# Optimization experiments

Hardware: AMD Instinct MI355X
Metric: run time of the kernel (lower is better)

Reference implementation:

```python
import jax, jax.numpy as jnp
import numpy as np
import math

B, T, D = 4, 4096, 512
K_CACHE = 16

def _layernorm(x, g, b, eps=1e-5):
    mu = x.mean(-1, keepdims=True)
    var = ((x - mu) ** 2).mean(-1, keepdims=True)
    return (x - mu) / jnp.sqrt(var + eps) * g + b

def _shift1(x):
    # prepend zero along time axis, drop last: x_prev[t] = x[t-1]
    return jnp.pad(x, ((0, 0), (1, 0), (0, 0)))[:, :-1]

def mipt_parallel_scan(p, theta, inp_re, inp_im):
    # Faithful replication of the torch loop: ceil(log2(T+1)) iterations,
    # each combining with the element shifted by ONE position (as written).
    Bt, Tt, Dt = p.shape
    a_re = (1.0 - p) * jnp.cos(theta)
    a_im = (1.0 - p) * jnp.sin(theta)
    b_re, b_im = inp_re, inp_im
    mask = (jnp.arange(Tt) >= 1)[None, :, None]
    steps = math.ceil(math.log2(Tt + 1))
    for _ in range(steps):
        ar_p, ai_p = _shift1(a_re), _shift1(a_im)
        br_p, bi_p = _shift1(b_re), _shift1(b_im)
        new_a_re = a_re * ar_p - a_im * ai_p
        new_a_im = a_re * ai_p + a_im * ar_p
        new_b_re = a_re * br_p - a_im * bi_p + b_re
        new_b_im = a_re * bi_p + a_im * br_p + b_im
        a_re = jnp.where(mask, new_a_re, a_re)
        a_im = jnp.where(mask, new_a_im, a_im)
        b_re = jnp.where(mask, new_b_re, b_re)
        b_im = jnp.where(mask, new_b_im, b_im)
    return b_re, b_im

def setup_inputs() -> dict:
    key = jax.random.key(0)
    ks = jax.random.split(key, 32)
    s = 0.02
    def W(k, i, o):
        return jax.random.normal(k, (i, o), jnp.float32) * s
    inp = {
        'x': jax.random.normal(ks[0], (B, T, D), jnp.float32),
        'ln1_g': jnp.ones((D,), jnp.float32), 'ln1_b': jnp.zeros((D,), jnp.float32),
        'ln2_g': jnp.ones((D,), jnp.float32), 'ln2_b': jnp.zeros((D,), jnp.float32),
        'Wp_w': W(ks[1], D, D), 'Wp_b': jnp.zeros((D,), jnp.float32),
        'Wt_w': W(ks[2], D, D), 'Wt_b': jnp.zeros((D,), jnp.float32),
        'Wr_w': W(ks[3], D, D), 'Wr_b': jnp.zeros((D,), jnp.float32),
        'Wi_w': W(ks[4], D, D), 'Wi_b': jnp.zeros((D,), jnp.float32),
        'Wk_w': W(ks[5], D, D), 'Wk_b': jnp.zeros((D,), jnp.float32),
        'Wv_w': W(ks[6], D, D), 'Wv_b': jnp.zeros((D,), jnp.float32),
        'Wq_w': W(ks[7], D, D), 'Wq_b': jnp.zeros((D,), jnp.float32),
        'gate_w': W(ks[8], D, 1), 'gate_b': jnp.zeros((1,), jnp.float32),
        'ffn1_w': W(ks[9], D, 4 * D), 'ffn1_b': jnp.zeros((4 * D,), jnp.float32),
        'ffn2_w': W(ks[10], 4 * D, D), 'ffn2_b': jnp.zeros((D,), jnp.float32),
    }
    return inp

def reference(x, ln1_g, ln1_b, ln2_g, ln2_b, Wp_w, Wp_b, Wt_w, Wt_b, Wr_w, Wr_b,
              Wi_w, Wi_b, Wk_w, Wk_b, Wv_w, Wv_b, Wq_w, Wq_b, gate_w, gate_b,
              ffn1_w, ffn1_b, ffn2_w, ffn2_b):
    Bx, Tx, Dx = x.shape
    residual = x
    xn = _layernorm(x, ln1_g, ln1_b)
    p = jax.nn.sigmoid(xn @ Wp_w + Wp_b)
    theta = xn @ Wt_w + Wt_b
    inp_re = xn @ Wr_w + Wr_b
    inp_im = xn @ Wi_w + Wi_b
    h_re, _h_im = mipt_parallel_scan(p, theta, inp_re, inp_im)
    h_mean = h_re.mean(axis=1)  # [B, D]
    # CausalSparseCache (eval mode)
    p_scalar = p.mean(axis=-1)  # [B, T]
    K = min(K_CACHE, Tx)
    _, topk_idx = jax.lax.top_k(p_scalar, K)  # [B, K]
    idx = jnp.broadcast_to(topk_idx[:, :, None], (Bx, K, Dx))
    h_topk = jnp.take_along_axis(h_re, idx, axis=1)  # [B, K, D]
    keys = h_topk @ Wk_w + Wk_b
    values = h_topk @ Wv_w + Wv_b
    query = (h_mean @ Wq_w + Wq_b)[:, None, :]  # [B, 1, D]
    scores = jnp.einsum('bqd,bkd->bqk', query, keys) / math.sqrt(Dx)
    attn = jax.nn.softmax(scores, axis=-1)
    cache_out = jnp.einsum('bqk,bkd->bqd', attn, values)[:, 0]  # [B, D]
    g = jax.nn.sigmoid(h_mean @ gate_w + gate_b)  # [B, 1]
    out = h_mean + g * cache_out
    h = h_re + residual
    hn = _layernorm(h, ln2_g, ln2_b)
    ffn = jax.nn.gelu(hn @ ffn1_w + ffn1_b, approximate=False) @ ffn2_w + ffn2_b
    h = h + ffn
    return (h, out)
```

## Files before the change

kernel.cpp:

```cpp
#include <hip/hip_runtime.h>
#include <hip/hip_bf16.h>
#include <cstdint>
#include <cstddef>

typedef __bf16 bf16;
typedef __attribute__((ext_vector_type(8))) __bf16 bf16x8;
typedef __attribute__((ext_vector_type(4))) float f32x4;

#define BB 4
#define TT 4096
#define DD 512
#define MM (BB * TT)
#define OUT1_OFF ((size_t)MM * DD)

typedef __attribute__((address_space(1))) void as1_void;
typedef __attribute__((address_space(3))) void as3_void;

__device__ __forceinline__ void gl_lds16(const void* g, void* l) {
    __builtin_amdgcn_global_load_lds((as1_void*)(uintptr_t)g,
                                     (as3_void*)(uintptr_t)l, 16, 0, 0);
}

__global__ void transpose_bf16(const float* __restrict__ in, bf16* __restrict__ out,
                               int R, int C) {
    __shared__ float tile[32][33];
    const int c0 = blockIdx.x * 32, r0 = blockIdx.y * 32;
    const int tx = threadIdx.x, ty = threadIdx.y;
#pragma unroll
    for (int i = 0; i < 32; i += 8)
        tile[ty + i][tx] = in[(size_t)(r0 + ty + i) * C + (c0 + tx)];
    __syncthreads();
#pragma unroll
    for (int i = 0; i < 32; i += 8)
        out[(size_t)(c0 + ty + i) * R + (r0 + tx)] = (bf16)tile[tx][ty + i];
}

__global__ void pack_bias(const float* __restrict__ a, const float* __restrict__ b,
                          const float* __restrict__ c, const float* __restrict__ d,
                          float* __restrict__ o) {
    const int i = blockIdx.x * 256 + threadIdx.x;
    if (i < 2048) {
        const float* s = (i < 512) ? a : (i < 1024) ? b : (i < 1536) ? c : d;
        o[i] = s[i & 511];
    }
}

__global__ void zero_kernel(float* __restrict__ p, int n) {
    const int i = blockIdx.x * 256 + threadIdx.x;
    if (i < n) p[i] = 0.f;
}

__global__ __launch_bounds__(256) void ln_kernel(
    const float* __restrict__ X, const float* __restrict__ Xadd,
    const float* __restrict__ gw, const float* __restrict__ bw,
    bf16* __restrict__ out) {
    const int row = blockIdx.x * 4 + (threadIdx.x >> 6);
    const int lane = threadIdx.x & 63;
    const float* xr = X + (size_t)row * DD + lane * 8;
    float v[8];
    float4 v0 = *(const float4*)xr;
    float4 v1 = *(const float4*)(xr + 4);
    v[0] = v0.x; v[1] = v0.y; v[2] = v0.z; v[3] = v0.w;
    v[4] = v1.x; v[5] = v1.y; v[6] = v1.z; v[7] = v1.w;
    if (Xadd) {
        const float* ad = Xadd + (size_t)row * DD + lane * 8;
        float4 a0 = *(const float4*)ad;
        float4 a1 = *(const float4*)(ad + 4);
        v[0] += a0.x; v[1] += a0.y; v[2] += a0.z; v[3] += a0.w;
        v[4] += a1.x; v[5] += a1.y; v[6] += a1.z; v[7] += a1.w;
    }
    float s = 0.f, ss = 0.f;
#pragma unroll
    for (int i = 0; i < 8; ++i) { s += v[i]; ss += v[i] * v[i]; }
#pragma unroll
    for (int o = 32; o; o >>= 1) { s += __shfl_down(s, o); ss += __shfl_down(ss, o); }
    s = __shfl(s, 0); ss = __shfl(ss, 0);
    const float mu = s * (1.f / DD);
    const float var = ss * (1.f / DD) - mu * mu;
    const float rstd = rsqrtf(var + 1e-5f);
    bf16x8 o8;
#pragma unroll
    for (int i = 0; i < 8; ++i)
        o8[i] = (bf16)((v[i] - mu) * rstd * gw[lane * 8 + i] + bw[lane * 8 + i]);
    *(bf16x8*)(out + (size_t)row * DD + lane * 8) = o8;
}

#define MF(a_, b_, c_) c_ = __builtin_amdgcn_mfma_f32_16x16x32_bf16(a_, b_, c_, 0, 0, 0)

template <int MODE>
__global__ __launch_bounds__(256) void gemm_bt(
    const bf16* __restrict__ A, const bf16* __restrict__ Bt,
    const float* __restrict__ bias, void* __restrict__ Cout,
    void* __restrict__ Cout2,
    const float* __restrict__ add1, const float* __restrict__ add2,
    int M, int N, int K) {
    __shared__ bf16 As[2][4096];
    __shared__ bf16 Bs[2][4096];
    const int tid = threadIdx.x;
    const int lane = tid & 63;
    const int wv = tid >> 6;
    const int wr = wv >> 1, wc = wv & 1;
    const int nb = N >> 7;
    const int nwg = gridDim.x;
    int bx = blockIdx.x;
    if ((nwg & 7) == 0) bx = (bx & 7) * (nwg >> 3) + (bx >> 3);
    const int bm = bx / nb, bn = bx % nb;
    const int m0 = bm << 7, n0 = bn << 7;

    const int srow = tid >> 2;
    const int scol = (((tid & 3) ^ ((tid >> 3) & 3)) << 3);
    const bf16* Asrc = A + (size_t)(m0 + srow) * K + scol;
    const bf16* Bsrc = Bt + (size_t)(n0 + srow) * K + scol;
    const size_t rstep = (size_t)64 * K;

    const int lr = lane & 15, lg = lane >> 4;
    const int sel = ((lg ^ ((lr >> 1) & 3)) << 3);
    const int aoff = (wr * 64 + lr) * 32 + sel;
    const int boff = (wc * 64 + lr) * 32 + sel;

#define STG(buf, k0)                                                \
    do {                                                            \
        gl_lds16(Asrc + (k0),         &As[buf][wv * 512]);          \
        gl_lds16(Asrc + (k0) + rstep, &As[buf][wv * 512 + 2048]);   \
        gl_lds16(Bsrc + (k0),         &Bs[buf][wv * 512]);          \
        gl_lds16(Bsrc + (k0) + rstep, &Bs[buf][wv * 512 + 2048]);   \
    } while (0)

    f32x4 acc00 = {}, acc01 = {}, acc02 = {}, acc03 = {};
    f32x4 acc10 = {}, acc11 = {}, acc12 = {}, acc13 = {};
    f32x4 acc20 = {}, acc21 = {}, acc22 = {}, acc23 = {};
    f32x4 acc30 = {}, acc31 = {}, acc32 = {}, acc33 = {};

    const int NT = K >> 5;
    STG(0, 0);
    STG(1, 32);
    for (int t = 0; t < NT; ++t) {
        if (t + 1 < NT) asm volatile("s_waitcnt vmcnt(4)" ::: "memory");
        else            asm volatile("s_waitcnt vmcnt(0)" ::: "memory");
        __builtin_amdgcn_s_barrier();
        asm volatile("" ::: "memory");
        const bf16* Ab = As[t & 1];
        const bf16* Bb = Bs[t & 1];
        bf16x8 af0 = *(const bf16x8*)&Ab[aoff];
        bf16x8 af1 = *(const bf16x8*)&Ab[aoff + 512];
        bf16x8 af2 = *(const bf16x8*)&Ab[aoff + 1024];
        bf16x8 af3 = *(const bf16x8*)&Ab[aoff + 1536];
        bf16x8 bf0 = *(const bf16x8*)&Bb[boff];
        bf16x8 bf1 = *(const bf16x8*)&Bb[boff + 512];
        bf16x8 bf2 = *(const bf16x8*)&Bb[boff + 1024];
        bf16x8 bf3 = *(const bf16x8*)&Bb[boff + 1536];
        MF(af0, bf0, acc00); MF(af0, bf1, acc01); MF(af0, bf2, acc02); MF(af0, bf3, acc03);
        MF(af1, bf0, acc10); MF(af1, bf1, acc11); MF(af1, bf2, acc12); MF(af1, bf3, acc13);
        MF(af2, bf0, acc20); MF(af2, bf1, acc21); MF(af2, bf2, acc22); MF(af2, bf3, acc23);
        MF(af3, bf0, acc30); MF(af3, bf1, acc31); MF(af3, bf2, acc32); MF(af3, bf3, acc33);
        __builtin_amdgcn_s_barrier();
        asm volatile("" ::: "memory");
        if (t + 2 < NT) STG(t & 1, (t + 2) << 5);
    }
#undef STG

#define EPI(mi, ni, ACC)                                                        \
    do {                                                                        \
        const int gmb = m0 + wr * 64 + mi * 16 + 4 * lg;                        \
        const int gn = n0 + wc * 64 + ni * 16 + lr;                             \
        const float bia = bias[gn];                                             \
        _Pragma("unroll")                                                       \
        for (int i = 0; i < 4; ++i) {                                           \
            float v = ACC[i] + bia;                                             \
            const int row = gmb + i;                                            \
            if (MODE == 0) {                                                    \
                if (gn < 512) ((float*)Cout)[(size_t)row * 512 + gn] = v;       \
                else ((bf16*)Cout2)[(size_t)row * 1536 + (gn - 512)] = (bf16)v; \
            } else if (MODE == 1) {                                             \
                const float ge = 0.5f * v * (1.0f + erff(v * 0.70710678118654752f)); \
                ((bf16*)Cout)[(size_t)row * N + gn] = (bf16)ge;                 \
            } else {                                                            \
                const size_t off = (size_t)row * N + gn;                        \
                ((float*)Cout)[off] = v + add1[off] + add2[off];                \
            }                                                                   \
        }                                                                       \
    } while (0)
    EPI(0, 0, acc00); EPI(0, 1, acc01); EPI(0, 2, acc02); EPI(0, 3, acc03);
    EPI(1, 0, acc10); EPI(1, 1, acc11); EPI(1, 2, acc12); EPI(1, 3, acc13);
    EPI(2, 0, acc20); EPI(2, 1, acc21); EPI(2, 2, acc22); EPI(2, 3, acc23);
    EPI(3, 0, acc30); EPI(3, 1, acc31); EPI(3, 2, acc32); EPI(3, 3, acc33);
#undef EPI
}

__global__ __launch_bounds__(256) void pscalar_kernel(const float* __restrict__ linp,
                                                      float* __restrict__ ps) {
    const int row = blockIdx.x * 4 + (threadIdx.x >> 6);
    const int lane = threadIdx.x & 63;
    const float* pr = linp + (size_t)row * 512 + lane * 8;
    float s = 0.f;
#pragma unroll
    for (int i = 0; i < 8; ++i) {
        const float v = pr[i];
        s += __builtin_amdgcn_rcpf(1.f + __expf(-v));
    }
#pragma unroll
    for (int o = 32; o; o >>= 1) s += __shfl_down(s, o);
    if (!lane) ps[row] = s * (1.f / 512.f);
}

#define SCL 16
__global__ __launch_bounds__(256) void scan_kernel(const float* __restrict__ linp,
                                                   const bf16* __restrict__ lint,
                                                   float* __restrict__ h_re) {
    const int blk = blockIdx.x;
    const int dh = blk & 1;
    const int tc = (blk >> 1) & 255;
    const int b = blk >> 9;
    const int d = dh * 256 + threadIdx.x;
    const int t0 = tc * SCL;

    float par[13], pai[13], pbr[13], pbi[13];
#pragma unroll
    for (int k = 0; k < 13; ++k) { par[k] = 0.f; pai[k] = 0.f; pbr[k] = 0.f; pbi[k] = 0.f; }

    const int warm = (tc == 0) ? 0 : 13;
    const float* pp = linp + (size_t)(b * TT + t0 - warm) * 512 + d;
    const bf16* tp = lint + (size_t)(b * TT + t0 - warm) * 1536 + d;
    float* pout = h_re + ((size_t)(b * TT + t0)) * DD + d;

#define XFORM(car, cai, cbr, cbi)                                        \
    const float pl = pp[0];                                              \
    const float th = (float)tp[0];                                       \
    const float re = (float)tp[512];                                     \
    const float im = (float)tp[1024];                                    \
    pp += 512; tp += 1536;                                               \
    const float om = __builtin_amdgcn_rcpf(1.f + __expf(pl));            \
    float fr_, sn, cs;                                                   \
    { const float rv_ = th * 0.15915494309189535f;                       \
      asm("v_fract_f32 %0, %1" : "=v"(fr_) : "v"(rv_));                  \
      asm("v_sin_f32 %0, %1" : "=v"(sn) : "v"(fr_));                     \
      asm("v_cos_f32 %0, %1" : "=v"(cs) : "v"(fr_)); }                   \
    float car = om * cs, cai = om * sn, cbr = re, cbi = im;

    for (int s = 0; s < warm; ++s) {
        XFORM(car, cai, cbr, cbi)
#pragma unroll
        for (int k = 0; k < 13; ++k) {
            const float tar = par[k], tai = pai[k], tbr = pbr[k], tbi = pbi[k];
            par[k] = car; pai[k] = cai; pbr[k] = cbr; pbi[k] = cbi;
            const float nbr = car * tbr - cai * tbi + cbr;
            const float nbi = car * tbi + cai * tbr + cbi;
            if (k < 12) {
                const float nar = car * tar - cai * tai;
                const float nai = car * tai + cai * tar;
                car = nar; cai = nai;
            }
            cbr = nbr; cbi = nbi;
        }
    }

#pragma unroll 4
    for (int s = 0; s < SCL; ++s) {
        const int t = t0 + s;
        XFORM(car, cai, cbr, cbi)
        if (t == 0) {
#pragma unroll
            for (int k = 0; k < 13; ++k) { par[k] = car; pai[k] = cai; pbr[k] = cbr; pbi[k] = cbi; }
        } else {
#pragma unroll
            for (int k = 0; k < 13; ++k) {
                const float tar = par[k], tai = pai[k], tbr = pbr[k], tbi = pbi[k];
                par[k] = car; pai[k] = cai; pbr[k] = cbr; pbi[k] = cbi;
                const float nbr = car * tbr - cai * tbi + cbr;
                const float nbi = car * tbi + cai * tbr + cbi;
                if (k < 12) {
                    const float nar = car * tar - cai * tai;
                    const float nai = car * tai + cai * tar;
                    car = nar; cai = nai;
                }
                cbr = nbr; cbi = nbi;
            }
        }
        pout[(size_t)s * DD] = cbr;
    }
#undef XFORM
}

__global__ __launch_bounds__(256) void hmean_kernel(const float* __restrict__ h_re,
                                                    float* __restrict__ hsum) {
    const int blk = blockIdx.x;
    const int b = blk >> 6;
    const int dh = (blk >> 5) & 1;
    const int tc = blk & 31;
    const int d = dh * 256 + threadIdx.x;
    float s = 0.f;
    const float* p = h_re + ((size_t)(b * TT + tc * 128)) * DD + d;
    for (int t = 0; t < 128; ++t) s += p[(size_t)t * DD];
    atomicAdd(&hsum[b * DD + d], s);
}

__global__ __launch_bounds__(256) void topk_kernel(const float* __restrict__ ps,
                                                   int* __restrict__ idx_out) {
    __shared__ float vals[TT];
    __shared__ float rv[4];
    __shared__ int ri[4];
    const int b = blockIdx.x, tid = threadIdx.x;
    for (int i = tid; i < TT; i += 256) vals[i] = ps[b * TT + i];
    __syncthreads();
    for (int kk = 0; kk < 16; ++kk) {
        float bv = -1e30f; int bi = 0x7fffffff;
        for (int i = tid; i < TT; i += 256) {
            const float v = vals[i];
            if (v > bv || (v == bv && i < bi)) { bv = v; bi = i; }
        }
#pragma unroll
        for (int o = 32; o; o >>= 1) {
            const float ov = __shfl_down(bv, o);
            const int oi = __shfl_down(bi, o);
            if (ov > bv || (ov == bv && oi < bi)) { bv = ov; bi = oi; }
        }
        const int lane = tid & 63, wid = tid >> 6;
        if (!lane) { rv[wid] = bv; ri[wid] = bi; }
        __syncthreads();
        if (!tid) {
            float fbv = rv[0]; int fbi = ri[0];
            for (int w = 1; w < 4; ++w)
                if (rv[w] > fbv || (rv[w] == fbv && ri[w] < fbi)) { fbv = rv[w]; fbi = ri[w]; }
            idx_out[b * 16 + kk] = fbi;
            vals[fbi] = -1e30f;
        }
        __syncthreads();
    }
}

__global__ __launch_bounds__(256) void kv_kernel(
    const float* __restrict__ h_re, const int* __restrict__ tki,
    const float* __restrict__ Wk, const float* __restrict__ Wkb,
    const float* __restrict__ Wv, const float* __restrict__ Wvb,
    float* __restrict__ keys, float* __restrict__ vals) {
    const int blk = blockIdx.x;
    const int b = blk >> 4, j = blk & 15;
    const int tid = threadIdx.x;
    __shared__ float hrow[512];
    const int row = tki[b * 16 + j];
    for (int i = tid; i < 512; i += 256)
        hrow[i] = h_re[((size_t)(b * TT + row)) * DD + i];
    __syncthreads();
    for (int n = tid; n < 512; n += 256) {
        float sk = Wkb[n], sv = Wvb[n];
        for (int k = 0; k < 512; ++k) {
            const float h = hrow[k];
            sk += h * Wk[(size_t)k * 512 + n];
            sv += h * Wv[(size_t)k * 512 + n];
        }
        keys[((size_t)(b * 16 + j)) * 512 + n] = sk;
        vals[((size_t)(b * 16 + j)) * 512 + n] = sv;
    }
}

__global__ __launch_bounds__(256) void attn_out_kernel(
    const float* __restrict__ hsum, const float* __restrict__ Wq,
    const float* __restrict__ Wqb, const float* __restrict__ gw,
    const float* __restrict__ gb, const float* __restrict__ keys,
    const float* __restrict__ vals, float* __restrict__ out1) {
    const int b = blockIdx.x, tid = threadIdx.x;
    const int lane = tid & 63, wid = tid >> 6;
    __shared__ float hm[512];
    __shared__ float q[512];
    __shared__ float sc[16];
    __shared__ float red[4];
    for (int d0 = tid; d0 < 512; d0 += 256)
        hm[d0] = hsum[b * 512 + d0] * (1.f / 4096.f);
    __syncthreads();
    for (int n = tid; n < 512; n += 256) {
        float s = Wqb[n];
        for (int k = 0; k < 512; ++k) s += hm[k] * Wq[(size_t)k * 512 + n];
        q[n] = s;
    }
    float gp = 0.f;
    for (int k = tid; k < 512; k += 256) gp += hm[k] * gw[k];
#pragma unroll
    for (int o = 32; o; o >>= 1) gp += __shfl_down(gp, o);
    if (!lane) red[wid] = gp;
    __syncthreads();
    const float g = 1.f / (1.f + __expf(-(red[0] + red[1] + red[2] + red[3] + gb[0])));
    for (int kk = wid; kk < 16; kk += 4) {
        float sp = 0.f;
        const float* kr = keys + ((size_t)(b * 16 + kk)) * 512;
        for (int k2 = lane; k2 < 512; k2 += 64) sp += q[k2] * kr[k2];
#pragma unroll
        for (int o = 32; o; o >>= 1) sp += __shfl_down(sp, o);
        if (!lane) sc[kk] = sp * 0.04419417382415922f;
    }
    __syncthreads();
    float mx = sc[0];
#pragma unroll
    for (int kk = 1; kk < 16; ++kk) mx = fmaxf(mx, sc[kk]);
    float den = 0.f;
    float w16[16];
#pragma unroll
    for (int kk = 0; kk < 16; ++kk) { w16[kk] = __expf(sc[kk] - mx); den += w16[kk]; }
    const float rden = 1.f / den;
    for (int d0 = tid; d0 < 512; d0 += 256) {
        float co = 0.f;
#pragma unroll
        for (int kk = 0; kk < 16; ++kk)
            co += w16[kk] * vals[((size_t)(b * 16 + kk)) * 512 + d0];
        out1[b * 512 + d0] = hm[d0] + g * (co * rden);
    }
}

extern "C" void kernel_launch(void* const* d_in, const int* in_sizes, int n_in,
                              void* d_out, int out_size, void* d_ws, size_t ws_size,
                              hipStream_t stream) {
    const float* x    = (const float*)d_in[0];
    const float* ln1g = (const float*)d_in[1];
    const float* ln1b = (const float*)d_in[2];
    const float* ln2g = (const float*)d_in[3];
    const float* ln2b = (const float*)d_in[4];
    const float* Wp_w = (const float*)d_in[5];
    const float* Wp_b = (const float*)d_in[6];
    const float* Wt_w = (const float*)d_in[7];
    const float* Wt_b = (const float*)d_in[8];
    const float* Wr_w = (const float*)d_in[9];
    const float* Wr_b = (const float*)d_in[10];
    const float* Wi_w = (const float*)d_in[11];
    const float* Wi_b = (const float*)d_in[12];
    const float* Wk_w = (const float*)d_in[13];
    const float* Wk_b = (const float*)d_in[14];
    const float* Wv_w = (const float*)d_in[15];
    const float* Wv_b = (const float*)d_in[16];
    const float* Wq_w = (const float*)d_in[17];
    const float* Wq_b = (const float*)d_in[18];
    const float* gw   = (const float*)d_in[19];
    const float* gb   = (const float*)d_in[20];
    const float* f1w  = (const float*)d_in[21];
    const float* f1b  = (const float*)d_in[22];
    const float* f2w  = (const float*)d_in[23];
    const float* f2b  = (const float*)d_in[24];

    char* wsp = (char*)d_ws;
    float* linp = (float*)wsp;
    bf16* lint = (bf16*)(wsp + 33554432);
    char* p = wsp + 83886080;
    float* h_re = (float*)p; p += 33554432;
    bf16* xn = (bf16*)p;     p += 16777216;
    bf16* hn = (bf16*)p;     p += 16777216;
    bf16* wcat = (bf16*)p;   p += 2097152;
    bf16* f1bt = (bf16*)p;   p += 2097152;
    bf16* f2bt = (bf16*)p;   p += 2097152;
    float* bcat = (float*)p; p += 8192;
    float* ps = (float*)p;   p += 65536;
    float* hsum = (float*)p; p += 8192;
    int* tki = (int*)p;      p += 256;
    float* keys = (float*)p; p += 131072;
    float* valsb = (float*)p;
    bf16* act = (bf16*)wsp;
    float* out0 = (float*)d_out;
    float* out1 = (float*)d_out + OUT1_OFF;

    dim3 tb(32, 8);
    transpose_bf16<<<dim3(16, 16), tb, 0, stream>>>(Wp_w, wcat + (size_t)0 * 512 * 512, 512, 512);
    transpose_bf16<<<dim3(16, 16), tb, 0, stream>>>(Wt_w, wcat + (size_t)1 * 512 * 512, 512, 512);
    transpose_bf16<<<dim3(16, 16), tb, 0, stream>>>(Wr_w, wcat + (size_t)2 * 512 * 512, 512, 512);
    transpose_bf16<<<dim3(16, 16), tb, 0, stream>>>(Wi_w, wcat + (size_t)3 * 512 * 512, 512, 512);
    transpose_bf16<<<dim3(64, 16), tb, 0, stream>>>(f1w, f1bt, 512, 2048);
    transpose_bf16<<<dim3(16, 64), tb, 0, stream>>>(f2w, f2bt, 2048, 512);
    pack_bias<<<8, 256, 0, stream>>>(Wp_b, Wt_b, Wr_b, Wi_b, bcat);

    ln_kernel<<<4096, 256, 0, stream>>>(x, nullptr, ln1g, ln1b, xn);
    gemm_bt<0><<<2048, 256, 0, stream>>>(xn, wcat, bcat, linp, lint, nullptr, nullptr, MM, 2048, 512);
    pscalar_kernel<<<4096, 256, 0, stream>>>(linp, ps);
    scan_kernel<<<2048, 256, 0, stream>>>(linp, lint, h_re);
    zero_kernel<<<8, 256, 0, stream>>>(hsum, 2048);
    hmean_kernel<<<256, 256, 0, stream>>>(h_re, hsum);
    topk_kernel<<<4, 256, 0, stream>>>(ps, tki);
    kv_kernel<<<64, 256, 0, stream>>>(h_re, tki, Wk_w, Wk_b, Wv_w, Wv_b, keys, valsb);
    attn_out_kernel<<<4, 256, 0, stream>>>(hsum, Wq_w, Wq_b, gw, gb, keys, valsb, out1);
    ln_kernel<<<4096, 256, 0, stream>>>(h_re, x, ln2g, ln2b, hn);
    gemm_bt<1><<<2048, 256, 0, stream>>>(hn, f1bt, f1b, act, nullptr, nullptr, nullptr, MM, 2048, 512);
    gemm_bt<2><<<512, 256, 0, stream>>>(act, f2bt, f2b, out0, nullptr, h_re, x, MM, 512, 2048);
}
```

Before: 428.2 us.

## Fuse sigmoid and p-mean into projection GEMM epilogue, interleave scan inputs

Result: faster. 419.5 us (-2.0%).

```diff
diff --git a/kernel.cpp b/kernel.cpp
--- a/kernel.cpp
+++ b/kernel.cpp
@@ -5,6 +5,7 @@
 
 typedef __bf16 bf16;
 typedef __attribute__((ext_vector_type(8))) __bf16 bf16x8;
+typedef __attribute__((ext_vector_type(4))) __bf16 bf16x4;
 typedef __attribute__((ext_vector_type(4))) float f32x4;
 
 #define BB 4
@@ -20,6 +21,8 @@
     __builtin_amdgcn_global_load_lds((as1_void*)(uintptr_t)g,
                                      (as3_void*)(uintptr_t)l, 16, 0, 0);
 }
+
+#define SIGM(x) (__builtin_amdgcn_rcpf(1.f + __expf(-(x))))
 
 __global__ void transpose_bf16(const float* __restrict__ in, bf16* __restrict__ out,
                                int R, int C) {
@@ -159,6 +162,58 @@
     }
 #undef STG
 
+    if constexpr (MODE == 0) {
+        const int cls = n0 >> 9;
+        if (cls == 0) {
+            const int pidx = (n0 + wc * 64) >> 6;
+#define EPI0(mi, A0, A1, A2, A3)                                              \
+    do {                                                                      \
+        const int gmb = m0 + wr * 64 + mi * 16 + 4 * lg;                      \
+        const int dbase = n0 + wc * 64 + lr;                                  \
+        const float b0_ = bias[dbase], b1_ = bias[dbase + 16],                \
+                    b2_ = bias[dbase + 32], b3_ = bias[dbase + 48];           \
+        _Pragma("unroll")                                                     \
+        for (int i = 0; i < 4; ++i) {                                         \
+            const int row = gmb + i;                                          \
+            const float p0 = SIGM(A0[i] + b0_);                               \
+            const float p1 = SIGM(A1[i] + b1_);                               \
+            const float p2 = SIGM(A2[i] + b2_);                               \
+            const float p3 = SIGM(A3[i] + b3_);                               \
+            bf16* ob = (bf16*)Cout + (size_t)row * 2048;                      \
+            ob[(size_t)dbase * 4]        = (bf16)(1.f - p0);                  \
+            ob[(size_t)(dbase + 16) * 4] = (bf16)(1.f - p1);                  \
+            ob[(size_t)(dbase + 32) * 4] = (bf16)(1.f - p2);                  \
+            ob[(size_t)(dbase + 48) * 4] = (bf16)(1.f - p3);                  \
+            float s_ = p0 + p1 + p2 + p3;                                     \
+            s_ += __shfl_xor(s_, 1); s_ += __shfl_xor(s_, 2);                 \
+            s_ += __shfl_xor(s_, 4); s_ += __shfl_xor(s_, 8);                 \
+            if (lr == 0) ((float*)Cout2)[(size_t)pidx * MM + row] = s_;       \
+        }                                                                     \
+    } while (0)
+            EPI0(0, acc00, acc01, acc02, acc03);
+            EPI0(1, acc10, acc11, acc12, acc13);
+            EPI0(2, acc20, acc21, acc22, acc23);
+            EPI0(3, acc30, acc31, acc32, acc33);
+#undef EPI0
+        } else {
+#define EPIS(mi, ni, ACC)                                                     \
+    do {                                                                      \
+        const int gmb = m0 + wr * 64 + mi * 16 + 4 * lg;                      \
+        const int gn = n0 + wc * 64 + ni * 16 + lr;                           \
+        const int dn = gn & 511;                                              \
+        const float bia = bias[gn];                                           \
+        _Pragma("unroll")                                                     \
+        for (int i = 0; i < 4; ++i)                                           \
+            ((bf16*)Cout)[((size_t)(gmb + i) * 512 + dn) * 4 + cls] =         \
+                (bf16)(ACC[i] + bia);                                         \
+    } while (0)
+            EPIS(0, 0, acc00); EPIS(0, 1, acc01); EPIS(0, 2, acc02); EPIS(0, 3, acc03);
+            EPIS(1, 0, acc10); EPIS(1, 1, acc11); EPIS(1, 2, acc12); EPIS(1, 3, acc13);
+            EPIS(2, 0, acc20); EPIS(2, 1, acc21); EPIS(2, 2, acc22); EPIS(2, 3, acc23);
+            EPIS(3, 0, acc30); EPIS(3, 1, acc31); EPIS(3, 2, acc32); EPIS(3, 3, acc33);
+#undef EPIS
+        }
+    } else {
 #define EPI(mi, ni, ACC)                                                        \
     do {                                                                        \
         const int gmb = m0 + wr * 64 + mi * 16 + 4 * lg;                        \
@@ -168,10 +223,7 @@
         for (int i = 0; i < 4; ++i) {                                           \
             float v = ACC[i] + bia;                                             \
             const int row = gmb + i;                                            \
-            if (MODE == 0) {                                                    \
-                if (gn < 512) ((float*)Cout)[(size_t)row * 512 + gn] = v;       \
-                else ((bf16*)Cout2)[(size_t)row * 1536 + (gn - 512)] = (bf16)v; \
-            } else if (MODE == 1) {                                             \
+            if (MODE == 1) {                                                    \
                 const float ge = 0.5f * v * (1.0f + erff(v * 0.70710678118654752f)); \
                 ((bf16*)Cout)[(size_t)row * N + gn] = (bf16)ge;                 \
             } else {                                                            \
@@ -180,37 +232,30 @@
             }                                                                   \
         }                                                                       \
     } while (0)
-    EPI(0, 0, acc00); EPI(0, 1, acc01); EPI(0, 2, acc02); EPI(0, 3, acc03);
-    EPI(1, 0, acc10); EPI(1, 1, acc11); EPI(1, 2, acc12); EPI(1, 3, acc13);
-    EPI(2, 0, acc20); EPI(2, 1, acc21); EPI(2, 2, acc22); EPI(2, 3, acc23);
-    EPI(3, 0, acc30); EPI(3, 1, acc31); EPI(3, 2, acc32); EPI(3, 3, acc33);
+        EPI(0, 0, acc00); EPI(0, 1, acc01); EPI(0, 2, acc02); EPI(0, 3, acc03);
+        EPI(1, 0, acc10); EPI(1, 1, acc11); EPI(1, 2, acc12); EPI(1, 3, acc13);
+        EPI(2, 0, acc20); EPI(2, 1, acc21); EPI(2, 2, acc22); EPI(2, 3, acc23);
+        EPI(3, 0, acc30); EPI(3, 1, acc31); EPI(3, 2, acc32); EPI(3, 3, acc33);
 #undef EPI
-}
-
-__global__ __launch_bounds__(256) void pscalar_kernel(const float* __restrict__ linp,
-                                                      float* __restrict__ ps) {
-    const int row = blockIdx.x * 4 + (threadIdx.x >> 6);
-    const int lane = threadIdx.x & 63;
-    const float* pr = linp + (size_t)row * 512 + lane * 8;
+    }
+}
+
+__global__ __launch_bounds__(256) void pscalar_fin(const float* __restrict__ part,
+                                                   float* __restrict__ ps) {
+    const int i = blockIdx.x * 256 + threadIdx.x;
     float s = 0.f;
 #pragma unroll
-    for (int i = 0; i < 8; ++i) {
-        const float v = pr[i];
-        s += __builtin_amdgcn_rcpf(1.f + __expf(-v));
-    }
-#pragma unroll
-    for (int o = 32; o; o >>= 1) s += __shfl_down(s, o);
-    if (!lane) ps[row] = s * (1.f / 512.f);
-}
-
-#define SCL 16
-__global__ __launch_bounds__(256) void scan_kernel(const float* __restrict__ linp,
-                                                   const bf16* __restrict__ lint,
+    for (int j = 0; j < 8; ++j) s += part[(size_t)j * MM + i];
+    ps[i] = s * (1.f / 512.f);
+}
+
+#define SCL 32
+__global__ __launch_bounds__(256) void scan_kernel(const bf16* __restrict__ lint4,
                                                    float* __restrict__ h_re) {
     const int blk = blockIdx.x;
     const int dh = blk & 1;
-    const int tc = (blk >> 1) & 255;
-    const int b = blk >> 9;
+    const int tc = (blk >> 1) & 127;
+    const int b = blk >> 8;
     const int d = dh * 256 + threadIdx.x;
     const int t0 = tc * SCL;
 
@@ -219,38 +264,38 @@
     for (int k = 0; k < 13; ++k) { par[k] = 0.f; pai[k] = 0.f; pbr[k] = 0.f; pbi[k] = 0.f; }
 
     const int warm = (tc == 0) ? 0 : 13;
-    const float* pp = linp + (size_t)(b * TT + t0 - warm) * 512 + d;
-    const bf16* tp = lint + (size_t)(b * TT + t0 - warm) * 1536 + d;
+    const bf16* tp = lint4 + ((size_t)(b * TT + t0 - warm) * 512 + d) * 4;
     float* pout = h_re + ((size_t)(b * TT + t0)) * DD + d;
 
 #define XFORM(car, cai, cbr, cbi)                                        \
-    const float pl = pp[0];                                              \
-    const float th = (float)tp[0];                                       \
-    const float re = (float)tp[512];                                     \
-    const float im = (float)tp[1024];                                    \
-    pp += 512; tp += 1536;                                               \
-    const float om = __builtin_amdgcn_rcpf(1.f + __expf(pl));            \
+    const bf16x4 q_ = *(const bf16x4*)tp;                                \
+    tp += 2048;                                                          \
+    const float om = (float)q_[0];                                       \
+    const float th = (float)q_[1];                                       \
+    const float cbr = (float)q_[2];                                      \
+    const float cbi = (float)q_[3];                                      \
     float fr_, sn, cs;                                                   \
     { const float rv_ = th * 0.15915494309189535f;                       \
       asm("v_fract_f32 %0, %1" : "=v"(fr_) : "v"(rv_));                  \
       asm("v_sin_f32 %0, %1" : "=v"(sn) : "v"(fr_));                     \
       asm("v_cos_f32 %0, %1" : "=v"(cs) : "v"(fr_)); }                   \
-    float car = om * cs, cai = om * sn, cbr = re, cbi = im;
+    float car = om * cs, cai = om * sn;
 
     for (int s = 0; s < warm; ++s) {
         XFORM(car, cai, cbr, cbi)
+        float br_ = cbr, bi_ = cbi;
 #pragma unroll
         for (int k = 0; k < 13; ++k) {
             const float tar = par[k], tai = pai[k], tbr = pbr[k], tbi = pbi[k];
-            par[k] = car; pai[k] = cai; pbr[k] = cbr; pbi[k] = cbi;
-            const float nbr = car * tbr - cai * tbi + cbr;
-            const float nbi = car * tbi + cai * tbr + cbi;
+            par[k] = car; pai[k] = cai; pbr[k] = br_; pbi[k] = bi_;
+            const float nbr = car * tbr - cai * tbi + br_;
+            const float nbi = car * tbi + cai * tbr + bi_;
             if (k < 12) {
                 const float nar = car * tar - cai * tai;
                 const float nai = car * tai + cai * tar;
                 car = nar; cai = nai;
             }
-            cbr = nbr; cbi = nbi;
+            br_ = nbr; bi_ = nbi;
         }
     }
 
@@ -258,25 +303,26 @@
     for (int s = 0; s < SCL; ++s) {
         const int t = t0 + s;
         XFORM(car, cai, cbr, cbi)
+        float br_ = cbr, bi_ = cbi;
         if (t == 0) {
 #pragma unroll
-            for (int k = 0; k < 13; ++k) { par[k] = car; pai[k] = cai; pbr[k] = cbr; pbi[k] = cbi; }
+            for (int k = 0; k < 13; ++k) { par[k] = car; pai[k] = cai; pbr[k] = br_; pbi[k] = bi_; }
         } else {
 #pragma unroll
             for (int k = 0; k < 13; ++k) {
                 const float tar = par[k], tai = pai[k], tbr = pbr[k], tbi = pbi[k];
-                par[k] = car; pai[k] = cai; pbr[k] = cbr; pbi[k] = cbi;
-                const float nbr = car * tbr - cai * tbi + cbr;
-                const float nbi = car * tbi + cai * tbr + cbi;
+                par[k] = car; pai[k] = cai; pbr[k] = br_; pbi[k] = bi_;
+                const float nbr = car * tbr - cai * tbi + br_;
+                const float nbi = car * tbi + cai * tbr + bi_;
                 if (k < 12) {
                     const float nar = car * tar - cai * tai;
                     const float nai = car * tai + cai * tar;
                     car = nar; cai = nai;
                 }
-                cbr = nbr; cbi = nbi;
+                br_ = nbr; bi_ = nbi;
             }
         }
-        pout[(size_t)s * DD] = cbr;
+        pout[(size_t)s * DD] = br_;
     }
 #undef XFORM
 }
@@ -435,9 +481,8 @@
     const float* f2b  = (const float*)d_in[24];
 
     char* wsp = (char*)d_ws;
-    float* linp = (float*)wsp;
-    bf16* lint = (bf16*)(wsp + 33554432);
-    char* p = wsp + 83886080;
+    bf16* lint4 = (bf16*)wsp;
+    char* p = wsp + 67108864;
     float* h_re = (float*)p; p += 33554432;
     bf16* xn = (bf16*)p;     p += 16777216;
     bf16* hn = (bf16*)p;     p += 16777216;
@@ -446,6 +491,7 @@
     bf16* f2bt = (bf16*)p;   p += 2097152;
     float* bcat = (float*)p; p += 8192;
     float* ps = (float*)p;   p += 65536;
+    float* pspart = (float*)p; p += 524288;
     float* hsum = (float*)p; p += 8192;
     int* tki = (int*)p;      p += 256;
     float* keys = (float*)p; p += 131072;
@@ -464,9 +510,9 @@
     pack_bias<<<8, 256, 0, stream>>>(Wp_b, Wt_b, Wr_b, Wi_b, bcat);
 
     ln_kernel<<<4096, 256, 0, stream>>>(x, nullptr, ln1g, ln1b, xn);
-    gemm_bt<0><<<2048, 256, 0, stream>>>(xn, wcat, bcat, linp, lint, nullptr, nullptr, MM, 2048, 512);
-    pscalar_kernel<<<4096, 256, 0, stream>>>(linp, ps);
-    scan_kernel<<<2048, 256, 0, stream>>>(linp, lint, h_re);
+    gemm_bt<0><<<2048, 256, 0, stream>>>(xn, wcat, bcat, lint4, pspart, nullptr, nullptr, MM, 2048, 512);
+    pscalar_fin<<<64, 256, 0, stream>>>(pspart, ps);
+    scan_kernel<<<1024, 256, 0, stream>>>(lint4, h_re);
     zero_kernel<<<8, 256, 0, stream>>>(hsum, 2048);
     hmean_kernel<<<256, 256, 0, stream>>>(h_re, hsum);
     topk_kernel<<<4, 256, 0, stream>>>(ps, tki);
```
